# Performance work log

Measured on AMD Instinct MI355X. Metric: run time of the kernel, lower is better.

The kernel has to match this reference:

```python
import jax, jax.numpy as jnp
import numpy as np

# Instant-NGP style multi-resolution hash grid encoding
L = 16          # n_levels
F = 2           # n_feat_per_entry
D = 3           # spatial dim
T = 2 ** 19     # hashmap entries per level
B = 2 ** 20     # number of query points
BASE_RES, MAX_RES = 16, 512
PRIMES = (1, 2654435761, 805459861)  # NGP spatial hash primes


def setup_inputs() -> dict:
    key = jax.random.key(0)
    k1, k2 = jax.random.split(key)
    xyz = jax.random.uniform(k1, (B, D), dtype=jnp.float32)  # points in [0,1)^3
    offsets = np.arange(L + 1, dtype=np.int32) * T            # len L+1, offsets[-1] = n_total_embed
    n_total = int(offsets[-1])
    embeddings = (jax.random.uniform(k2, (n_total, F), dtype=jnp.float32) * 2.0 - 1.0) * 1e-4
    growth = np.exp(np.log(MAX_RES / BASE_RES) / (L - 1))
    resolutions = np.floor(BASE_RES * growth ** np.arange(L)).astype(np.int32)  # len L
    return {
        "xyz": xyz,
        "embeddings": embeddings,
        "offsets": jnp.asarray(offsets),
        "resolutions": jnp.asarray(resolutions),
        "min_xyz": jnp.zeros((D,), jnp.float32),
        "max_xyz": jnp.ones((D,), jnp.float32),
    }


def _encode(xyz, embeddings, offsets, resolutions, min_xyz, max_xyz):
    Bn, Dn = xyz.shape
    n_grid = 2 ** Dn  # corners of a cell
    # normalize to [0,1]; points outside the box are zeroed (valid mask)
    u = (xyz - min_xyz) / (max_xyz - min_xyz)                      # (B,D)
    valid = jnp.all((u >= 0.0) & (u <= 1.0), axis=-1)              # (B,)
    res = resolutions.astype(xyz.dtype)                            # (L,)
    pos = u[:, None, :] * res[None, :, None]                       # (B,L,D)
    pos0 = jnp.clip(jnp.floor(pos), 0.0, res[None, :, None] - 1.0) # lower cell corner
    frac = pos - pos0                                              # (B,L,D) in [0,1]
    # all 2^D corner offsets, bit d of corner c
    bits = jnp.asarray([[(c >> d) & 1 for d in range(Dn)] for c in range(n_grid)])  # (2^D, D)
    corners = pos0[:, :, None, :].astype(jnp.uint32) + bits[None, None].astype(jnp.uint32)  # (B,L,2^D,D)
    # trilinear weights: prod_d (frac if bit else 1-frac)
    fb = frac[:, :, None, :]
    w = jnp.prod(jnp.where(bits[None, None].astype(bool), fb, 1.0 - fb), axis=-1)  # (B,L,2^D)
    # spatial hash: xor of coord_d * prime_d (uint32 wraparound), mod level table size
    primes = jnp.asarray(PRIMES[:Dn], dtype=jnp.uint32)
    hp = corners * primes                                          # (B,L,2^D,D) uint32
    h = hp[..., 0]
    for d in range(1, Dn):
        h = h ^ hp[..., d]
    sizes = (offsets[1:] - offsets[:-1]).astype(jnp.uint32)        # (L,)
    idx = (h % sizes[None, :, None]).astype(jnp.int32) + offsets[:-1][None, :, None]  # (B,L,2^D)
    gathered = embeddings[idx]                                     # (B,L,2^D,F)
    out = jnp.einsum("blc,blcf->blf", w, gathered)                 # (B,L,F)
    out = out * valid[:, None, None].astype(out.dtype)
    return out.reshape(Bn, -1)                                     # (B, L*F)


def reference(xyz, embeddings, offsets, resolutions, min_xyz, max_xyz):
    return _encode(xyz, embeddings, offsets, resolutions, min_xyz, max_xyz)
```

## Files before the change

### kernel.cpp

```cpp
#include <hip/hip_runtime.h>

#define NLVL 16
#define NDENSE 7
#define PREPASS_CAP 600000

typedef float f32x2 __attribute__((ext_vector_type(2)));
typedef float f32x4 __attribute__((ext_vector_type(4)));
typedef _Float16 f16x2 __attribute__((ext_vector_type(2)));
typedef unsigned u32x2 __attribute__((ext_vector_type(2)));

__device__ __forceinline__ unsigned hash3(unsigned x, unsigned y, unsigned z) {
    return x ^ (y * 2654435761u) ^ (z * 805459861u);
}

__device__ __forceinline__ unsigned dense_total(const int* __restrict__ resolutions,
                                                unsigned doff[NDENSE]) {
    unsigned acc = 0;
    for (int ll = 0; ll < NDENSE; ++ll) {
        unsigned S = (unsigned)resolutions[ll] + 1u;
        doff[ll] = acc;
        acc += S * S * S;
    }
    return acc;
}

__global__ __launch_bounds__(256) void convert_fp16_kernel(
    const float* __restrict__ emb,
    _Float16*    __restrict__ htab,
    int n_entries)
{
    int i = blockIdx.x * 256 + (int)threadIdx.x;
    if (i >= n_entries) return;
    f32x2 v = reinterpret_cast<const f32x2*>(emb)[i];
    f16x2 h;
    h.x = (_Float16)v.x;
    h.y = (_Float16)v.y;
    reinterpret_cast<f16x2*>(htab)[i] = h;
}

__global__ __launch_bounds__(256) void densify_kernel(
    const float* __restrict__ emb,
    const int*   __restrict__ offsets,
    const int*   __restrict__ resolutions,
    float*       __restrict__ dense)
{
    unsigned doff[NDENSE];
    unsigned total = dense_total(resolutions, doff);
    if (total > PREPASS_CAP) total = PREPASS_CAP;
    unsigned tid = blockIdx.x * 256u + threadIdx.x;
    if (tid >= total) return;
    int l = 0;
    while (l < NDENSE - 1 && tid >= doff[l + 1]) ++l;
    unsigned idx = tid - doff[l];
    unsigned S = (unsigned)resolutions[l] + 1u;
    unsigned x = idx % S;
    unsigned t = idx / S;
    unsigned y = t % S;
    unsigned z = t / S;
    unsigned off  = (unsigned)offsets[l];
    unsigned size = (unsigned)offsets[l + 1] - off;
    unsigned mask = size - 1u;
    unsigned h = hash3(x, y, z);
    unsigned hm = ((size & mask) == 0u) ? (h & mask) : (h % size);
    const f32x2* src = reinterpret_cast<const f32x2*>(emb) + off + hm;
    f32x2* dst = reinterpret_cast<f32x2*>(dense) + tid;
    *dst = *src;
}

__global__ __launch_bounds__(256) void encode_kernel(
    const float* __restrict__ xyz,
    const float* __restrict__ emb,
    const _Float16* __restrict__ htab,
    const int*   __restrict__ offsets,
    const int*   __restrict__ resolutions,
    const float* __restrict__ min_xyz,
    const float* __restrict__ max_xyz,
    const float* __restrict__ dense,
    float*       __restrict__ scratch,
    float*       __restrict__ out,
    int B, int use_dense, int use_scratch, int use_fp16)
{
    const int g = blockIdx.x & 15;
    const int chunk = blockIdx.x >> 4;
    const int l = (g < 8) ? (8 + g) : (((g - 8) + (chunk >> 6)) & 7);
    const int p = chunk * 256 + (int)threadIdx.x;
    if (p >= B) return;

    const float res = (float)resolutions[l];
    const unsigned off  = (unsigned)offsets[l];
    const unsigned size = (unsigned)offsets[l + 1] - off;
    const unsigned mask = size - 1u;
    const bool pow2 = (size & mask) == 0u;
    const float mn0 = min_xyz[0], mn1 = min_xyz[1], mn2 = min_xyz[2];
    const float mx0 = max_xyz[0], mx1 = max_xyz[1], mx2 = max_xyz[2];

    const float x = xyz[p * 3 + 0];
    const float y = xyz[p * 3 + 1];
    const float z = xyz[p * 3 + 2];
    const float ux = (x - mn0) / (mx0 - mn0);
    const float uy = (y - mn1) / (mx1 - mn1);
    const float uz = (z - mn2) / (mx2 - mn2);
    const bool valid = (ux >= 0.0f) & (ux <= 1.0f) &
                       (uy >= 0.0f) & (uy <= 1.0f) &
                       (uz >= 0.0f) & (uz <= 1.0f);

    const float rm1 = res - 1.0f;
    const float px = ux * res, py = uy * res, pz = uz * res;
    const float p0x = fminf(fmaxf(floorf(px), 0.0f), rm1);
    const float p0y = fminf(fmaxf(floorf(py), 0.0f), rm1);
    const float p0z = fminf(fmaxf(floorf(pz), 0.0f), rm1);
    const float fx = px - p0x, fy = py - p0y, fz = pz - p0z;
    const float gx = 1.0f - fx, gy = 1.0f - fy, gz = 1.0f - fz;
    const unsigned cx0 = (unsigned)p0x;
    const unsigned cy0 = (unsigned)p0y;
    const unsigned cz0 = (unsigned)p0z;

    const unsigned P1 = 2654435761u;
    const unsigned P2 = 805459861u;

    float o0 = 0.0f, o1 = 0.0f;

    bool dense_ok = false;
    unsigned doff[NDENSE];
    if (use_dense && l < NDENSE) {
        unsigned total = dense_total(resolutions, doff);
        dense_ok = (total <= PREPASS_CAP);
    }

    if (dense_ok) {
        const unsigned S = (unsigned)resolutions[l] + 1u;
        const f32x2* lvl = reinterpret_cast<const f32x2*>(dense) + doff[l];
        const unsigned base = cx0 + S * (cy0 + S * cz0);
        f32x4 e00, e10, e01, e11;
        __builtin_memcpy(&e00, lvl + base,             16);
        __builtin_memcpy(&e10, lvl + base + S,         16);
        __builtin_memcpy(&e01, lvl + base + S * S,     16);
        __builtin_memcpy(&e11, lvl + base + S * S + S, 16);
        o0 += (gx * gy * gz) * e00.x;  o1 += (gx * gy * gz) * e00.y;
        o0 += (fx * gy * gz) * e00.z;  o1 += (fx * gy * gz) * e00.w;
        o0 += (gx * fy * gz) * e10.x;  o1 += (gx * fy * gz) * e10.y;
        o0 += (fx * fy * gz) * e10.z;  o1 += (fx * fy * gz) * e10.w;
        o0 += (gx * gy * fz) * e01.x;  o1 += (gx * gy * fz) * e01.y;
        o0 += (fx * gy * fz) * e01.z;  o1 += (fx * gy * fz) * e01.w;
        o0 += (gx * fy * fz) * e11.x;  o1 += (gx * fy * fz) * e11.y;
        o0 += (fx * fy * fz) * e11.z;  o1 += (fx * fy * fz) * e11.w;
    } else if (use_fp16 && pow2) {
        const unsigned* lvl32 = reinterpret_cast<const unsigned*>(htab) + off;
        const u32x2*    lvlp  = reinterpret_cast<const u32x2*>(lvl32);
        unsigned m4[4], h0a[4];
        u32x2 pr[4];
#pragma unroll
        for (int pi = 0; pi < 4; ++pi) {
            unsigned by = (unsigned)(pi & 1);
            unsigned bz = (unsigned)(pi >> 1);
            unsigned m = ((cy0 + by) * P1) ^ ((cz0 + bz) * P2);
            unsigned h0 = (cx0 ^ m) & mask;
            m4[pi] = m; h0a[pi] = h0;
            pr[pi] = lvlp[h0 >> 1];
        }
        unsigned e0b[4], e1b[4];
        if ((cx0 & 1u) == 0u) {
#pragma unroll
            for (int pi = 0; pi < 4; ++pi) {
                bool hi = (h0a[pi] & 1u) != 0u;
                e0b[pi] = hi ? pr[pi].y : pr[pi].x;
                e1b[pi] = hi ? pr[pi].x : pr[pi].y;
            }
        } else {
#pragma unroll
            for (int pi = 0; pi < 4; ++pi) {
                unsigned h1 = ((cx0 + 1u) ^ m4[pi]) & mask;
                e1b[pi] = lvl32[h1];
                e0b[pi] = (h0a[pi] & 1u) ? pr[pi].y : pr[pi].x;
            }
        }
#pragma unroll
        for (int pi = 0; pi < 4; ++pi) {
            unsigned by = (unsigned)(pi & 1);
            unsigned bz = (unsigned)(pi >> 1);
            float wy = by ? fy : gy;
            float wz = bz ? fz : gz;
            float wyz = wy * wz;
            f16x2 e0 = __builtin_bit_cast(f16x2, e0b[pi]);
            f16x2 e1 = __builtin_bit_cast(f16x2, e1b[pi]);
            float w0 = gx * wyz;
            float w1 = fx * wyz;
            o0 += w0 * (float)e0.x;  o1 += w0 * (float)e0.y;
            o0 += w1 * (float)e1.x;  o1 += w1 * (float)e1.y;
        }
    } else {
        const f32x2* lvl = reinterpret_cast<const f32x2*>(emb) + off;
#pragma unroll
        for (int c = 0; c < 8; ++c) {
            unsigned bx = (unsigned)(c & 1);
            unsigned by = (unsigned)((c >> 1) & 1);
            unsigned bz = (unsigned)((c >> 2) & 1);
            unsigned h = hash3(cx0 + bx, cy0 + by, cz0 + bz);
            unsigned hm = pow2 ? (h & mask) : (h % size);
            f32x2 e = lvl[hm];
            float w = (bx ? fx : gx) * (by ? fy : gy);
            w = w * (bz ? fz : gz);
            o0 += w * e.x;
            o1 += w * e.y;
        }
    }

    if (!valid) { o0 = 0.0f; o1 = 0.0f; }
    if (use_scratch) {
        f16x2 h; h.x = (_Float16)o0; h.y = (_Float16)o1;
        unsigned hb = __builtin_bit_cast(unsigned, h);
        unsigned* op = reinterpret_cast<unsigned*>(scratch) + (size_t)l * B + p;
        __builtin_nontemporal_store(hb, op);
    } else {
        f32x2 r; r.x = o0; r.y = o1;
        f32x2* op = reinterpret_cast<f32x2*>(out + (size_t)p * (NLVL * 2) + l * 2);
        __builtin_nontemporal_store(r, op);
    }
}

__global__ __launch_bounds__(256) void transpose_kernel(
    const float* __restrict__ scratch,
    float*       __restrict__ out,
    int B)
{
    __shared__ float tile[64][33];
    const int p0 = blockIdx.x * 64;
    const int tid = (int)threadIdx.x;

    const unsigned* src = reinterpret_cast<const unsigned*>(scratch);
#pragma unroll
    for (int k = 0; k < 4; ++k) {
        int it = tid + k * 256;
        int l  = it >> 6;
        int pi = it & 63;
        int p  = p0 + pi;
        unsigned vb = (p < B) ? src[(size_t)l * B + p] : 0u;
        f16x2 v = __builtin_bit_cast(f16x2, vb);
        tile[pi][2 * l]     = (float)v.x;
        tile[pi][2 * l + 1] = (float)v.y;
    }
    __syncthreads();

    const int pl = tid >> 2;
    const int q  = tid & 3;
    const int p  = p0 + pl;
    if (p >= B) return;
    float vals[8];
#pragma unroll
    for (int j = 0; j < 8; ++j) vals[j] = tile[pl][q * 8 + j];
    f32x4 lo, hi;
    lo.x = vals[0]; lo.y = vals[1]; lo.z = vals[2]; lo.w = vals[3];
    hi.x = vals[4]; hi.y = vals[5]; hi.z = vals[6]; hi.w = vals[7];
    f32x4* dst = reinterpret_cast<f32x4*>(out + (size_t)p * 32 + q * 8);
    __builtin_nontemporal_store(lo, dst);
    __builtin_nontemporal_store(hi, dst + 1);
}

extern "C" void kernel_launch(void* const* d_in, const int* in_sizes, int n_in,
                              void* d_out, int out_size, void* d_ws, size_t ws_size,
                              hipStream_t stream) {
    const float* xyz        = (const float*)d_in[0];
    const float* embeddings = (const float*)d_in[1];
    const int*   offsets    = (const int*)d_in[2];
    const int*   resolutions= (const int*)d_in[3];
    const float* min_xyz    = (const float*)d_in[4];
    const float* max_xyz    = (const float*)d_in[5];
    float* out = (float*)d_out;

    int B = in_sizes[0] / 3;
    int n_entries = in_sizes[1] / 2;

    size_t scratch_bytes = (size_t)B * NLVL * 4;
    size_t dense_bytes   = (size_t)PREPASS_CAP * 8;
    size_t htab_bytes    = (size_t)n_entries * 4;

    int use_scratch = (ws_size >= scratch_bytes + dense_bytes) ? 1 : 0;
    size_t dense_off = use_scratch ? scratch_bytes : 0;
    int use_dense = (ws_size >= dense_off + dense_bytes) ? 1 : 0;
    size_t htab_off = dense_off + (use_dense ? dense_bytes : 0);
    int use_fp16 = (ws_size >= htab_off + htab_bytes) ? 1 : 0;

    float*    scratch = (float*)d_ws;
    float*    dense_p = (float*)((char*)d_ws + dense_off);
    _Float16* htab    = (_Float16*)((char*)d_ws + htab_off);

    if (use_fp16) {
        int cgrid = (n_entries + 255) / 256;
        convert_fp16_kernel<<<cgrid, 256, 0, stream>>>(embeddings, htab, n_entries);
    }
    if (use_dense) {
        int pgrid = (PREPASS_CAP + 255) / 256;
        densify_kernel<<<pgrid, 256, 0, stream>>>(
            embeddings, offsets, resolutions, dense_p);
    }
    int nchunks = (B + 255) / 256;
    int grid = nchunks * NLVL;
    encode_kernel<<<grid, 256, 0, stream>>>(
        xyz, embeddings, htab, offsets, resolutions, min_xyz, max_xyz,
        dense_p, scratch, out, B, use_dense, use_scratch, use_fp16);
    if (use_scratch) {
        int tgrid = (B + 63) / 64;
        transpose_kernel<<<tgrid, 256, 0, stream>>>(scratch, out, B);
    }
}
```

Before: 428.1 us.

## Replace dense fp32 prepass with per-cell fp16 4-corner bricked table

The dense prepass for coarse levels now stores, for each cell, the four fp16 corner entries of a z-slice packed into 16 bytes, built from the fp16 table. The encode kernel needs two 16-byte loads per point instead of four, and the gathered data is half the size. This cuts memory traffic for levels 0-6, at the cost of a larger prepass buffer (16 bytes per cell), a prepass that runs after the fp16 conversion, and fp16 precision on the dense path.

New measurement: 417.1 us. 1.03x faster.

```diff
diff --git a/kernel.cpp b/kernel.cpp
--- a/kernel.cpp
+++ b/kernel.cpp
@@ -2,7 +2,7 @@
 
 #define NLVL 16
 #define NDENSE 7
-#define PREPASS_CAP 600000
+#define BDENSE_CAP 600000
 
 typedef float f32x2 __attribute__((ext_vector_type(2)));
 typedef float f32x4 __attribute__((ext_vector_type(4)));
@@ -13,13 +13,13 @@
     return x ^ (y * 2654435761u) ^ (z * 805459861u);
 }
 
-__device__ __forceinline__ unsigned dense_total(const int* __restrict__ resolutions,
-                                                unsigned doff[NDENSE]) {
+__device__ __forceinline__ unsigned bdense_total(const int* __restrict__ resolutions,
+                                                 unsigned bdoff[NDENSE]) {
     unsigned acc = 0;
     for (int ll = 0; ll < NDENSE; ++ll) {
-        unsigned S = (unsigned)resolutions[ll] + 1u;
-        doff[ll] = acc;
-        acc += S * S * S;
+        unsigned R = (unsigned)resolutions[ll];
+        bdoff[ll] = acc;
+        acc += R * R * (R + 1u);
     }
     return acc;
 }
@@ -38,33 +38,49 @@
     reinterpret_cast<f16x2*>(htab)[i] = h;
 }
 
-__global__ __launch_bounds__(256) void densify_kernel(
-    const float* __restrict__ emb,
-    const int*   __restrict__ offsets,
-    const int*   __restrict__ resolutions,
-    float*       __restrict__ dense)
+__global__ __launch_bounds__(256) void bdensify_kernel(
+    const unsigned* __restrict__ htab32,
+    const int*      __restrict__ offsets,
+    const int*      __restrict__ resolutions,
+    unsigned*       __restrict__ bdense)
 {
-    unsigned doff[NDENSE];
-    unsigned total = dense_total(resolutions, doff);
-    if (total > PREPASS_CAP) total = PREPASS_CAP;
+    unsigned bdoff[NDENSE];
+    unsigned total = bdense_total(resolutions, bdoff);
+    if (total > BDENSE_CAP) total = BDENSE_CAP;
     unsigned tid = blockIdx.x * 256u + threadIdx.x;
     if (tid >= total) return;
     int l = 0;
-    while (l < NDENSE - 1 && tid >= doff[l + 1]) ++l;
-    unsigned idx = tid - doff[l];
-    unsigned S = (unsigned)resolutions[l] + 1u;
-    unsigned x = idx % S;
-    unsigned t = idx / S;
-    unsigned y = t % S;
-    unsigned z = t / S;
+    while (l < NDENSE - 1 && tid >= bdoff[l + 1]) ++l;
+    unsigned idx = tid - bdoff[l];
+    unsigned R = (unsigned)resolutions[l];
+    unsigned cx = idx % R;
+    unsigned t  = idx / R;
+    unsigned cy = t % R;
+    unsigned z  = t / R;
     unsigned off  = (unsigned)offsets[l];
     unsigned size = (unsigned)offsets[l + 1] - off;
     unsigned mask = size - 1u;
-    unsigned h = hash3(x, y, z);
-    unsigned hm = ((size & mask) == 0u) ? (h & mask) : (h % size);
-    const f32x2* src = reinterpret_cast<const f32x2*>(emb) + off + hm;
-    f32x2* dst = reinterpret_cast<f32x2*>(dense) + tid;
-    *dst = *src;
+    bool pow2 = (size & mask) == 0u;
+    const unsigned* src = htab32 + off;
+
+    unsigned q[4];
+    {
+        unsigned h = hash3(cx,      cy,      z);
+        q[0] = src[pow2 ? (h & mask) : (h % size)];
+    }
+    {
+        unsigned h = hash3(cx + 1u, cy,      z);
+        q[1] = src[pow2 ? (h & mask) : (h % size)];
+    }
+    {
+        unsigned h = hash3(cx,      cy + 1u, z);
+        q[2] = src[pow2 ? (h & mask) : (h % size)];
+    }
+    {
+        unsigned h = hash3(cx + 1u, cy + 1u, z);
+        q[3] = src[pow2 ? (h & mask) : (h % size)];
+    }
+    __builtin_memcpy(bdense + (size_t)tid * 4u, q, 16);
 }
 
 __global__ __launch_bounds__(256) void encode_kernel(
@@ -75,10 +91,10 @@
     const int*   __restrict__ resolutions,
     const float* __restrict__ min_xyz,
     const float* __restrict__ max_xyz,
-    const float* __restrict__ dense,
+    const unsigned* __restrict__ bdense,
     float*       __restrict__ scratch,
     float*       __restrict__ out,
-    int B, int use_dense, int use_scratch, int use_fp16)
+    int B, int use_bdense, int use_scratch, int use_fp16)
 {
     const int g = blockIdx.x & 15;
     const int chunk = blockIdx.x >> 4;
@@ -120,30 +136,35 @@
 
     float o0 = 0.0f, o1 = 0.0f;
 
-    bool dense_ok = false;
-    unsigned doff[NDENSE];
-    if (use_dense && l < NDENSE) {
-        unsigned total = dense_total(resolutions, doff);
-        dense_ok = (total <= PREPASS_CAP);
-    }
-
-    if (dense_ok) {
-        const unsigned S = (unsigned)resolutions[l] + 1u;
-        const f32x2* lvl = reinterpret_cast<const f32x2*>(dense) + doff[l];
-        const unsigned base = cx0 + S * (cy0 + S * cz0);
-        f32x4 e00, e10, e01, e11;
-        __builtin_memcpy(&e00, lvl + base,             16);
-        __builtin_memcpy(&e10, lvl + base + S,         16);
-        __builtin_memcpy(&e01, lvl + base + S * S,     16);
-        __builtin_memcpy(&e11, lvl + base + S * S + S, 16);
-        o0 += (gx * gy * gz) * e00.x;  o1 += (gx * gy * gz) * e00.y;
-        o0 += (fx * gy * gz) * e00.z;  o1 += (fx * gy * gz) * e00.w;
-        o0 += (gx * fy * gz) * e10.x;  o1 += (gx * fy * gz) * e10.y;
-        o0 += (fx * fy * gz) * e10.z;  o1 += (fx * fy * gz) * e10.w;
-        o0 += (gx * gy * fz) * e01.x;  o1 += (gx * gy * fz) * e01.y;
-        o0 += (fx * gy * fz) * e01.z;  o1 += (fx * gy * fz) * e01.w;
-        o0 += (gx * fy * fz) * e11.x;  o1 += (gx * fy * fz) * e11.y;
-        o0 += (fx * fy * fz) * e11.z;  o1 += (fx * fy * fz) * e11.w;
+    bool bdense_ok = false;
+    unsigned bdoff[NDENSE];
+    if (use_bdense && l < NDENSE) {
+        unsigned total = bdense_total(resolutions, bdoff);
+        bdense_ok = (total <= BDENSE_CAP);
+    }
+
+    if (bdense_ok) {
+        const unsigned R = (unsigned)resolutions[l];
+        const unsigned base = bdoff[l] + (cz0 * R + cy0) * R + cx0;
+        unsigned q0[4], q1[4];
+        __builtin_memcpy(q0, bdense + (size_t)base * 4u, 16);
+        __builtin_memcpy(q1, bdense + (size_t)(base + R * R) * 4u, 16);
+        f16x2 e0 = __builtin_bit_cast(f16x2, q0[0]);
+        f16x2 e1 = __builtin_bit_cast(f16x2, q0[1]);
+        f16x2 e2 = __builtin_bit_cast(f16x2, q0[2]);
+        f16x2 e3 = __builtin_bit_cast(f16x2, q0[3]);
+        f16x2 e4 = __builtin_bit_cast(f16x2, q1[0]);
+        f16x2 e5 = __builtin_bit_cast(f16x2, q1[1]);
+        f16x2 e6 = __builtin_bit_cast(f16x2, q1[2]);
+        f16x2 e7 = __builtin_bit_cast(f16x2, q1[3]);
+        o0 += (gx * gy * gz) * (float)e0.x;  o1 += (gx * gy * gz) * (float)e0.y;
+        o0 += (fx * gy * gz) * (float)e1.x;  o1 += (fx * gy * gz) * (float)e1.y;
+        o0 += (gx * fy * gz) * (float)e2.x;  o1 += (gx * fy * gz) * (float)e2.y;
+        o0 += (fx * fy * gz) * (float)e3.x;  o1 += (fx * fy * gz) * (float)e3.y;
+        o0 += (gx * gy * fz) * (float)e4.x;  o1 += (gx * gy * fz) * (float)e4.y;
+        o0 += (fx * gy * fz) * (float)e5.x;  o1 += (fx * gy * fz) * (float)e5.y;
+        o0 += (gx * fy * fz) * (float)e6.x;  o1 += (gx * fy * fz) * (float)e6.y;
+        o0 += (fx * fy * fz) * (float)e7.x;  o1 += (fx * fy * fz) * (float)e7.y;
     } else if (use_fp16 && pow2) {
         const unsigned* lvl32 = reinterpret_cast<const unsigned*>(htab) + off;
         const u32x2*    lvlp  = reinterpret_cast<const u32x2*>(lvl32);
@@ -271,33 +292,33 @@
     int n_entries = in_sizes[1] / 2;
 
     size_t scratch_bytes = (size_t)B * NLVL * 4;
-    size_t dense_bytes   = (size_t)PREPASS_CAP * 8;
     size_t htab_bytes    = (size_t)n_entries * 4;
-
-    int use_scratch = (ws_size >= scratch_bytes + dense_bytes) ? 1 : 0;
-    size_t dense_off = use_scratch ? scratch_bytes : 0;
-    int use_dense = (ws_size >= dense_off + dense_bytes) ? 1 : 0;
-    size_t htab_off = dense_off + (use_dense ? dense_bytes : 0);
+    size_t bdense_bytes  = (size_t)BDENSE_CAP * 16;
+
+    int use_scratch = (ws_size >= scratch_bytes) ? 1 : 0;
+    size_t htab_off = use_scratch ? scratch_bytes : 0;
     int use_fp16 = (ws_size >= htab_off + htab_bytes) ? 1 : 0;
+    size_t bdense_off = htab_off + (use_fp16 ? htab_bytes : 0);
+    int use_bdense = (use_fp16 && ws_size >= bdense_off + bdense_bytes) ? 1 : 0;
 
     float*    scratch = (float*)d_ws;
-    float*    dense_p = (float*)((char*)d_ws + dense_off);
     _Float16* htab    = (_Float16*)((char*)d_ws + htab_off);
+    unsigned* bdense  = (unsigned*)((char*)d_ws + bdense_off);
 
     if (use_fp16) {
         int cgrid = (n_entries + 255) / 256;
         convert_fp16_kernel<<<cgrid, 256, 0, stream>>>(embeddings, htab, n_entries);
     }
-    if (use_dense) {
-        int pgrid = (PREPASS_CAP + 255) / 256;
-        densify_kernel<<<pgrid, 256, 0, stream>>>(
-            embeddings, offsets, resolutions, dense_p);
+    if (use_bdense) {
+        int pgrid = (BDENSE_CAP + 255) / 256;
+        bdensify_kernel<<<pgrid, 256, 0, stream>>>(
+            (const unsigned*)htab, offsets, resolutions, bdense);
     }
     int nchunks = (B + 255) / 256;
     int grid = nchunks * NLVL;
     encode_kernel<<<grid, 256, 0, stream>>>(
         xyz, embeddings, htab, offsets, resolutions, min_xyz, max_xyz,
-        dense_p, scratch, out, B, use_dense, use_scratch, use_fp16);
+        bdense, scratch, out, B, use_bdense, use_scratch, use_fp16);
     if (use_scratch) {
         int tgrid = (B + 63) / 64;
         transpose_kernel<<<tgrid, 256, 0, stream>>>(scratch, out, B);
```
